# Kernel optimization log

Hardware: AMD Instinct MI355X
Metric: run time of the kernel (lower is better)

## Reference

```python
import jax, jax.numpy as jnp
import numpy as np

B, C, H, W = 8, 64, 256, 256
M1, M2 = 32, 32  # kept Fourier modes per corner (n_modes//2)
EPS = 1e-5


def _gn(x):
    # GroupNorm(1, C): normalize over (C, H, W) per sample, biased variance
    mu = jnp.mean(x, axis=(1, 2, 3), keepdims=True)
    var = jnp.var(x, axis=(1, 2, 3), keepdims=True)
    return (x - mu) * jax.lax.rsqrt(var + EPS)


def setup_inputs() -> dict:
    key = jax.random.key(0)
    ks = jax.random.split(key, 12)
    spec_scale = 1.0 / (C * C)
    n = lambda k, shape, s=1.0: jax.random.normal(k, shape, dtype=jnp.float32) * s
    return dict(
        x=n(ks[0], (B, C, H, W)),
        t=n(ks[1], (B, C, 1)),
        w1r=n(ks[2], (C, C, M1, M2), spec_scale),
        w1i=n(ks[3], (C, C, M1, M2), spec_scale),
        w2r=n(ks[4], (C, C, M1, M2), spec_scale),
        w2i=n(ks[5], (C, C, M1, M2), spec_scale),
        norm1_w=jnp.ones((C,), jnp.float32),
        norm1_b=jnp.zeros((C,), jnp.float32),
        mlp_w1=n(ks[6], (C // 2, C), 0.05),
        mlp_b1=jnp.zeros((C // 2,), jnp.float32),
        mlp_w2=n(ks[7], (C, C // 2), 0.05),
        mlp_b2=jnp.zeros((C,), jnp.float32),
        gamma_w=n(ks[8], (C, C), 0.05),
        gamma_b=jnp.ones((C,), jnp.float32),
        beta_w=n(ks[9], (C, C), 0.05),
        beta_b=jnp.zeros((C,), jnp.float32),
    )


def reference(x, t, w1r, w1i, w2r, w2i, norm1_w, norm1_b,
              mlp_w1, mlp_b1, mlp_w2, mlp_b2,
              gamma_w, gamma_b, beta_w, beta_b):
    gelu = lambda v: jax.nn.gelu(v, approximate=False)  # torch exact gelu
    skip1 = x
    skip2 = gelu(x)

    # --- SpectralConv: rfft2 -> mode-truncated complex contraction -> irfft2 ---
    xf = jnp.fft.rfftn(x, axes=(2, 3))  # (B, C, H, W//2+1) complex
    b1 = jnp.einsum('bixy,ioxy->boxy', xf[:, :, :M1, :M2], w1r + 1j * w1i)
    b2 = jnp.einsum('bixy,ioxy->boxy', xf[:, :, -M1:, :M2], w2r + 1j * w2i)
    of = (jnp.zeros(xf.shape, xf.dtype)
          .at[:, :, :M1, :M2].set(b1)
          .at[:, :, -M1:, :M2].set(b2))
    y = jnp.fft.irfftn(of, s=(H, W), axes=(2, 3)).astype(x.dtype)

    # norm1 (GroupNorm(1,C) affine) + residual, gelu
    y = _gn(y) * norm1_w[None, :, None, None] + norm1_b[None, :, None, None]
    y = gelu(y + skip1)

    # pointwise MLP (Conv1d 1x1 chain == channel matmuls)
    h = gelu(jnp.einsum('oc,bcxy->boxy', mlp_w1, y) + mlp_b1[None, :, None, None])
    y = jnp.einsum('oc,bcxy->boxy', mlp_w2, h) + mlp_b2[None, :, None, None]

    # timeCondIN: FiLM gamma/beta from t via 1x1 Conv1d, non-affine GroupNorm(1,C)
    gamma = (jnp.einsum('oc,bcl->bol', gamma_w, t) + gamma_b[None, :, None])[..., None]
    beta = (jnp.einsum('oc,bcl->bol', beta_w, t) + beta_b[None, :, None])[..., None]
    y = gamma * _gn(y) + beta

    return y + skip2
```

## Files before the change

kernel.cpp:

```cpp
#include <hip/hip_runtime.h>
#include <math.h>

#define NB 8
#define NC 64
#define NH 256
#define NW 256
#define NHW 65536
#define NM 32
#define NPS 4194304
#define GN_EPS 1e-5f
#define OMEGA 0.0245436926061703f

typedef short shortx8 __attribute__((ext_vector_type(8)));
typedef float floatx4 __attribute__((ext_vector_type(4)));

__device__ __forceinline__ float gelu_f(float v) {
    return 0.5f * v * (1.0f + erff(v * 0.7071067811865475f));
}

__device__ __forceinline__ unsigned short f2bf(float f) {
    unsigned u = __builtin_bit_cast(unsigned, f);
    u = (u + 0x7fffu + ((u >> 16) & 1u)) >> 16;
    return (unsigned short)u;
}

__device__ __forceinline__ float bf2f(unsigned short u) {
    return __builtin_bit_cast(float, ((unsigned)u) << 16);
}

__global__ void k0_init(const float* __restrict__ t_in,
                        const float* __restrict__ gamma_w, const float* __restrict__ gamma_b,
                        const float* __restrict__ beta_w, const float* __restrict__ beta_b,
                        const float* __restrict__ mlp_w1, const float* __restrict__ mlp_w2,
                        float* __restrict__ gn_acc, float* __restrict__ gamma_bc,
                        float* __restrict__ beta_bc,
                        unsigned short* __restrict__ w1p_h, unsigned short* __restrict__ w1p_l,
                        unsigned short* __restrict__ w2p_h, unsigned short* __restrict__ w2p_l) {
    int t = threadIdx.x;
    if (t < 32) gn_acc[t] = 0.f;
    for (int idx = t; idx < NB * NC; idx += 256) {
        int b = idx >> 6, o = idx & 63;
        float g = gamma_b[o], be = beta_b[o];
        for (int c = 0; c < NC; ++c) {
            float tv = t_in[b * NC + c];
            g += gamma_w[o * NC + c] * tv;
            be += beta_w[o * NC + c] * tv;
        }
        gamma_bc[idx] = g;
        beta_bc[idx] = be;
    }
    for (int idx = t; idx < 2048; idx += 256) {
        float wv1 = mlp_w1[idx];
        unsigned short h1 = f2bf(wv1);
        w1p_h[idx] = h1;
        w1p_l[idx] = f2bf(wv1 - bf2f(h1));
        float wv2 = mlp_w2[idx];
        unsigned short h2 = f2bf(wv2);
        w2p_h[idx] = h2;
        w2p_l[idx] = f2bf(wv2 - bf2f(h2));
    }
}

__global__ __launch_bounds__(256) void k_tw(unsigned short* __restrict__ t1h,
                                            unsigned short* __restrict__ t1l,
                                            unsigned short* __restrict__ uh,
                                            unsigned short* __restrict__ ul,
                                            unsigned short* __restrict__ m2h,
                                            unsigned short* __restrict__ m2l,
                                            unsigned short* __restrict__ m4h,
                                            unsigned short* __restrict__ m4l) {
    int idx = blockIdx.x * 256 + threadIdx.x;
    if (idx < 16384) {
        int n = idx >> 8, w = idx & 255;
        float ph = OMEGA * (float)(((n & 31) * w) & 255);
        float s, c;
        sincosf(ph, &s, &c);
        float v = (n < 32) ? c : -s;
        unsigned short h = f2bf(v);
        t1h[idx] = h;
        t1l[idx] = f2bf(v - bf2f(h));

        int w2 = idx >> 6, k = idx & 63;
        int k31 = k & 31;
        float m = (k31 == 0) ? 1.f : 2.f;
        float ph2 = OMEGA * (float)((k31 * w2) & 255);
        sincosf(ph2, &s, &c);
        float v2 = (k < 32) ? m * c : -m * s;
        h = f2bf(v2);
        uh[idx] = h;
        ul[idx] = f2bf(v2 - bf2f(h));
    }
    {
        int m = idx >> 9, k = idx & 511;
        int j = m & 63;
        int f = (j < 32) ? j : 192 + j;
        int h256 = k & 255;
        float s, c;
        sincosf(OMEGA * (float)((f * h256) & 255), &s, &c);
        float v = (m < 64) ? ((k < 256) ? c : s) : ((k < 256) ? -s : c);
        unsigned short hh = f2bf(v);
        m2h[idx] = hh;
        m2l[idx] = f2bf(v - bf2f(hh));
    }
    {
        const float sc = 1.0f / 65536.0f;
        int m = idx >> 7, k = idx & 127;
        int h256 = m & 255;
        int j = k & 63;
        int f = (j < 32) ? j : 192 + j;
        float s, c;
        sincosf(OMEGA * (float)((f * h256) & 255), &s, &c);
        float v = ((m < 256) ? ((k < 64) ? c : -s) : ((k < 64) ? s : c)) * sc;
        unsigned short hh = f2bf(v);
        m4h[idx] = hh;
        m4l[idx] = f2bf(v - bf2f(hh));
    }
}

__global__ __launch_bounds__(256, 4) void k1_dftw(const float* __restrict__ x,
                                                  const unsigned short* __restrict__ t1h,
                                                  const unsigned short* __restrict__ t1l,
                                                  float* __restrict__ xw_re,
                                                  float* __restrict__ xw_im) {
    __shared__ unsigned short a_h[128 * 72];
    __shared__ unsigned short a_l[128 * 72];
    int blk = blockIdx.x;
    int bc = blk >> 1;
    int h0 = (blk & 1) * 128;
    const float* src = x + (size_t)bc * NHW + (size_t)h0 * NW;
    int t = threadIdx.x;
    int lane = t & 63, wv = t >> 6, lm = lane & 15, lg = lane >> 4;

    floatx4 acc[2][4] = {};
#pragma unroll
    for (int ks = 0; ks < 4; ++ks) {
        if (ks) __syncthreads();
        for (int i = t; i < 2048; i += 256) {
            int r = i >> 4;
            int c4 = (i & 15) << 2;
            float4 v = *(const float4*)&src[(size_t)r * NW + (ks << 6) + c4];
            int off = r * 72 + c4;
            ushort4 h4, l4;
            h4.x = f2bf(v.x); l4.x = f2bf(v.x - bf2f(h4.x));
            h4.y = f2bf(v.y); l4.y = f2bf(v.y - bf2f(h4.y));
            h4.z = f2bf(v.z); l4.z = f2bf(v.z - bf2f(h4.z));
            h4.w = f2bf(v.w); l4.w = f2bf(v.w - bf2f(h4.w));
            *(ushort4*)&a_h[off] = h4;
            *(ushort4*)&a_l[off] = l4;
        }
        __syncthreads();
#pragma unroll
        for (int kk = 0; kk < 2; ++kk) {
            shortx8 ah[2], al[2], bh[4], bl[4];
#pragma unroll
            for (int mt = 0; mt < 2; ++mt) {
                int off = (wv * 32 + mt * 16 + lm) * 72 + kk * 32 + lg * 8;
                ah[mt] = *(const shortx8*)&a_h[off];
                al[mt] = *(const shortx8*)&a_l[off];
            }
#pragma unroll
            for (int nt = 0; nt < 4; ++nt) {
                int off = (nt * 16 + lm) * 256 + ks * 64 + kk * 32 + lg * 8;
                bh[nt] = *(const shortx8*)&t1h[off];
                bl[nt] = *(const shortx8*)&t1l[off];
            }
#pragma unroll
            for (int mt = 0; mt < 2; ++mt)
#pragma unroll
                for (int nt = 0; nt < 4; ++nt) {
                    acc[mt][nt] = __builtin_amdgcn_mfma_f32_16x16x32_bf16(ah[mt], bh[nt], acc[mt][nt], 0, 0, 0);
                    acc[mt][nt] = __builtin_amdgcn_mfma_f32_16x16x32_bf16(ah[mt], bl[nt], acc[mt][nt], 0, 0, 0);
                    acc[mt][nt] = __builtin_amdgcn_mfma_f32_16x16x32_bf16(al[mt], bh[nt], acc[mt][nt], 0, 0, 0);
                }
        }
    }
    size_t rowg = (size_t)bc * NH + h0;
#pragma unroll
    for (int mt = 0; mt < 2; ++mt)
#pragma unroll
        for (int nt = 0; nt < 4; ++nt) {
            int n = nt * 16 + lm;
            float* dst = (n < 32) ? xw_re : xw_im;
            int kx = n & 31;
#pragma unroll
            for (int r = 0; r < 4; ++r) {
                int row = wv * 32 + mt * 16 + lg * 4 + r;
                dst[(rowg + row) * NM + kx] = acc[mt][nt][r];
            }
        }
}

__global__ __launch_bounds__(256, 2) void k2_dfth(const float* __restrict__ xw_re,
                                                  const float* __restrict__ xw_im,
                                                  const unsigned short* __restrict__ m2h,
                                                  const unsigned short* __restrict__ m2l,
                                                  float* __restrict__ xf_re,
                                                  float* __restrict__ xf_im) {
    __shared__ unsigned short bt_h[32 * 520];
    __shared__ unsigned short bt_l[32 * 520];
    int bc = blockIdx.x;
    size_t base = (size_t)bc * (NH * NM);
    int t = threadIdx.x;
    for (int idx4 = t; idx4 < 2048; idx4 += 256) {
        int h = idx4 >> 3;
        int kxg = (idx4 & 7) << 2;
        float4 vr = ((const float4*)(xw_re + base))[idx4];
        float4 vi = ((const float4*)(xw_im + base))[idx4];
        float fr[4] = {vr.x, vr.y, vr.z, vr.w};
        float fi[4] = {vi.x, vi.y, vi.z, vi.w};
#pragma unroll
        for (int q = 0; q < 4; ++q) {
            int rowo = (kxg + q) * 520;
            unsigned short hh = f2bf(fr[q]);
            bt_h[rowo + h] = hh;
            bt_l[rowo + h] = f2bf(fr[q] - bf2f(hh));
            hh = f2bf(fi[q]);
            bt_h[rowo + 256 + h] = hh;
            bt_l[rowo + 256 + h] = f2bf(fi[q] - bf2f(hh));
        }
    }
    __syncthreads();

    int lane = t & 63, wv = t >> 6, lm = lane & 15, lg = lane >> 4;
    floatx4 acc[2][2] = {};
#pragma unroll
    for (int ks = 0; ks < 16; ++ks) {
        shortx8 bh[2], bl[2], ah[2], al[2];
#pragma unroll
        for (int nt = 0; nt < 2; ++nt) {
            int off = (nt * 16 + lm) * 520 + ks * 32 + lg * 8;
            bh[nt] = *(const shortx8*)&bt_h[off];
            bl[nt] = *(const shortx8*)&bt_l[off];
        }
#pragma unroll
        for (int mt = 0; mt < 2; ++mt) {
            int off = (wv * 32 + mt * 16 + lm) * 512 + ks * 32 + lg * 8;
            ah[mt] = *(const shortx8*)&m2h[off];
            al[mt] = *(const shortx8*)&m2l[off];
        }
#pragma unroll
        for (int mt = 0; mt < 2; ++mt)
#pragma unroll
            for (int nt = 0; nt < 2; ++nt) {
                acc[mt][nt] = __builtin_amdgcn_mfma_f32_16x16x32_bf16(ah[mt], bh[nt], acc[mt][nt], 0, 0, 0);
                acc[mt][nt] = __builtin_amdgcn_mfma_f32_16x16x32_bf16(ah[mt], bl[nt], acc[mt][nt], 0, 0, 0);
                acc[mt][nt] = __builtin_amdgcn_mfma_f32_16x16x32_bf16(al[mt], bh[nt], acc[mt][nt], 0, 0, 0);
            }
    }
    size_t ob = (size_t)bc * 2048;
#pragma unroll
    for (int mt = 0; mt < 2; ++mt)
#pragma unroll
        for (int nt = 0; nt < 2; ++nt) {
            int n = nt * 16 + lm;
#pragma unroll
            for (int r = 0; r < 4; ++r) {
                int row = wv * 32 + mt * 16 + lg * 4 + r;
                float* dst = (row < 64) ? xf_re : xf_im;
                dst[ob + (row & 63) * 32 + n] = acc[mt][nt][r];
            }
        }
}

__global__ __launch_bounds__(256) void k3_mix(const float* __restrict__ xf_re,
                                              const float* __restrict__ xf_im,
                                              const float* __restrict__ w1r, const float* __restrict__ w1i,
                                              const float* __restrict__ w2r, const float* __restrict__ w2i,
                                              float* __restrict__ yf_re, float* __restrict__ yf_im) {
    __shared__ float xr_l[4 * 64 * 32];
    __shared__ float xi_l[4 * 64 * 32];
    int blk = blockIdx.x;
    int bh = blk & 1;
    int oct = (blk >> 1) & 7;
    int ky = blk >> 4;
    for (int idx = threadIdx.x; idx < 4 * 64 * 32; idx += 256) {
        int bb = idx >> 11;
        int i = (idx >> 5) & 63;
        int kx = idx & 31;
        size_t g = ((size_t)((bh * 4 + bb) * 64 + i) * 64 + ky) * 32 + kx;
        xr_l[idx] = xf_re[g];
        xi_l[idx] = xf_im[g];
    }
    __syncthreads();
    const float* wr = (ky < 32) ? w1r : w2r;
    const float* wi = (ky < 32) ? w1i : w2i;
    int kyl = ky & 31;
    int t = threadIdx.x;
    int kx = t & 31, oo = t >> 5;
    int o = oct * 8 + oo;
    float accr[4] = {0.f, 0.f, 0.f, 0.f};
    float acci[4] = {0.f, 0.f, 0.f, 0.f};
    for (int i = 0; i < 64; ++i) {
        size_t wbase = ((size_t)(i * 64 + o) * 32 + kyl) * 32 + kx;
        float wrv = wr[wbase];
        float wiv = wi[wbase];
#pragma unroll
        for (int bb = 0; bb < 4; ++bb) {
            float xr = xr_l[(bb * 64 + i) * 32 + kx];
            float xi = xi_l[(bb * 64 + i) * 32 + kx];
            accr[bb] += xr * wrv - xi * wiv;
            acci[bb] += xr * wiv + xi * wrv;
        }
    }
#pragma unroll
    for (int bb = 0; bb < 4; ++bb) {
        int b = bh * 4 + bb;
        size_t g = ((size_t)(b * 64 + o) * 64 + ky) * 32 + kx;
        yf_re[g] = accr[bb];
        yf_im[g] = acci[bb];
    }
}

__global__ __launch_bounds__(256, 2) void k4_idfth(const float* __restrict__ yf_re,
                                                   const float* __restrict__ yf_im,
                                                   const unsigned short* __restrict__ m4h,
                                                   const unsigned short* __restrict__ m4l,
                                                   float* __restrict__ yh_re,
                                                   float* __restrict__ yh_im) {
    __shared__ unsigned short bt_h[32 * 136];
    __shared__ unsigned short bt_l[32 * 136];
    int bc = blockIdx.x;
    size_t base = (size_t)bc * 2048;
    int t = threadIdx.x;
    for (int idx4 = t; idx4 < 512; idx4 += 256) {
        int j = idx4 >> 3;
        int kxg = (idx4 & 7) << 2;
        float4 vr = ((const float4*)(yf_re + base))[idx4];
        float4 vi = ((const float4*)(yf_im + base))[idx4];
        float fr[4] = {vr.x, vr.y, vr.z, vr.w};
        float fi[4] = {vi.x, vi.y, vi.z, vi.w};
#pragma unroll
        for (int q = 0; q < 4; ++q) {
            int rowo = (kxg + q) * 136;
            unsigned short hh = f2bf(fr[q]);
            bt_h[rowo + j] = hh;
            bt_l[rowo + j] = f2bf(fr[q] - bf2f(hh));
            hh = f2bf(fi[q]);
            bt_h[rowo + 64 + j] = hh;
            bt_l[rowo + 64 + j] = f2bf(fi[q] - bf2f(hh));
        }
    }
    __syncthreads();

    int lane = t & 63, wv = t >> 6, lm = lane & 15, lg = lane >> 4;
    floatx4 acc[8][2] = {};
#pragma unroll
    for (int ks = 0; ks < 4; ++ks) {
        shortx8 bh[2], bl[2];
#pragma unroll
        for (int nt = 0; nt < 2; ++nt) {
            int off = (nt * 16 + lm) * 136 + ks * 32 + lg * 8;
            bh[nt] = *(const shortx8*)&bt_h[off];
            bl[nt] = *(const shortx8*)&bt_l[off];
        }
#pragma unroll
        for (int mt = 0; mt < 8; ++mt) {
            int off = (wv * 128 + mt * 16 + lm) * 128 + ks * 32 + lg * 8;
            shortx8 ah = *(const shortx8*)&m4h[off];
            shortx8 al = *(const shortx8*)&m4l[off];
#pragma unroll
            for (int nt = 0; nt < 2; ++nt) {
                acc[mt][nt] = __builtin_amdgcn_mfma_f32_16x16x32_bf16(ah, bh[nt], acc[mt][nt], 0, 0, 0);
                acc[mt][nt] = __builtin_amdgcn_mfma_f32_16x16x32_bf16(ah, bl[nt], acc[mt][nt], 0, 0, 0);
                acc[mt][nt] = __builtin_amdgcn_mfma_f32_16x16x32_bf16(al, bh[nt], acc[mt][nt], 0, 0, 0);
            }
        }
    }
    size_t ob = (size_t)bc * (NH * NM);
#pragma unroll
    for (int mt = 0; mt < 8; ++mt)
#pragma unroll
        for (int nt = 0; nt < 2; ++nt) {
            int n = nt * 16 + lm;
#pragma unroll
            for (int r = 0; r < 4; ++r) {
                int row = wv * 128 + mt * 16 + lg * 4 + r;
                float* dst = (row < 256) ? yh_re : yh_im;
                dst[ob + (row & 255) * 32 + n] = acc[mt][nt][r];
            }
        }
}

__global__ __launch_bounds__(256, 2) void k5_irfftw(const float* __restrict__ yh_re,
                                                    const float* __restrict__ yh_im,
                                                    const unsigned short* __restrict__ uh,
                                                    const unsigned short* __restrict__ ul,
                                                    float* __restrict__ yout,
                                                    float* __restrict__ gn_acc) {
    __shared__ unsigned short a_h[128 * 72];
    __shared__ unsigned short a_l[128 * 72];
    __shared__ float red[8];
    int blk = blockIdx.x;
    size_t row0 = (size_t)blk * 128;
    int t = threadIdx.x;

    for (int i = t; i < 1024; i += 256) {
        int r = i >> 3;
        int c4 = (i & 7) << 2;
        float4 vr = *(const float4*)&yh_re[(row0 + r) * NM + c4];
        float4 vi = *(const float4*)&yh_im[(row0 + r) * NM + c4];
        int offr = r * 72 + c4;
        ushort4 h4, l4;
        h4.x = f2bf(vr.x); l4.x = f2bf(vr.x - bf2f(h4.x));
        h4.y = f2bf(vr.y); l4.y = f2bf(vr.y - bf2f(h4.y));
        h4.z = f2bf(vr.z); l4.z = f2bf(vr.z - bf2f(h4.z));
        h4.w = f2bf(vr.w); l4.w = f2bf(vr.w - bf2f(h4.w));
        *(ushort4*)&a_h[offr] = h4;
        *(ushort4*)&a_l[offr] = l4;
        h4.x = f2bf(vi.x); l4.x = f2bf(vi.x - bf2f(h4.x));
        h4.y = f2bf(vi.y); l4.y = f2bf(vi.y - bf2f(h4.y));
        h4.z = f2bf(vi.z); l4.z = f2bf(vi.z - bf2f(h4.z));
        h4.w = f2bf(vi.w); l4.w = f2bf(vi.w - bf2f(h4.w));
        *(ushort4*)&a_h[offr + 32] = h4;
        *(ushort4*)&a_l[offr + 32] = l4;
    }
    __syncthreads();

    int lane = t & 63, wv = t >> 6, lm = lane & 15, lg = lane >> 4;
    floatx4 acc[2][16] = {};
#pragma unroll
    for (int kk = 0; kk < 2; ++kk) {
        shortx8 ah[2], al[2];
#pragma unroll
        for (int mt = 0; mt < 2; ++mt) {
            int off = (wv * 32 + mt * 16 + lm) * 72 + kk * 32 + lg * 8;
            ah[mt] = *(const shortx8*)&a_h[off];
            al[mt] = *(const shortx8*)&a_l[off];
        }
#pragma unroll
        for (int nt = 0; nt < 16; ++nt) {
            int w = nt * 16 + lm;
            shortx8 bh = *(const shortx8*)&uh[w * 64 + kk * 32 + lg * 8];
            shortx8 bl = *(const shortx8*)&ul[w * 64 + kk * 32 + lg * 8];
#pragma unroll
            for (int mt = 0; mt < 2; ++mt) {
                acc[mt][nt] = __builtin_amdgcn_mfma_f32_16x16x32_bf16(ah[mt], bh, acc[mt][nt], 0, 0, 0);
                acc[mt][nt] = __builtin_amdgcn_mfma_f32_16x16x32_bf16(ah[mt], bl, acc[mt][nt], 0, 0, 0);
                acc[mt][nt] = __builtin_amdgcn_mfma_f32_16x16x32_bf16(al[mt], bh, acc[mt][nt], 0, 0, 0);
            }
        }
    }

    float sum = 0.f, sq = 0.f;
#pragma unroll
    for (int mt = 0; mt < 2; ++mt)
#pragma unroll
        for (int nt = 0; nt < 16; ++nt) {
            int w = nt * 16 + lm;
#pragma unroll
            for (int r = 0; r < 4; ++r) {
                int row = wv * 32 + mt * 16 + lg * 4 + r;
                float v = acc[mt][nt][r];
                yout[(row0 + row) * NW + w] = v;
                sum += v;
                sq += v * v;
            }
        }
#pragma unroll
    for (int off = 32; off > 0; off >>= 1) {
        sum += __shfl_down(sum, off);
        sq += __shfl_down(sq, off);
    }
    if (lane == 0) { red[wv] = sum; red[4 + wv] = sq; }
    __syncthreads();
    if (t == 0) {
        int b = blk >> 7;
        atomicAdd(&gn_acc[b * 4 + 0], red[0] + red[1] + red[2] + red[3]);
        atomicAdd(&gn_acc[b * 4 + 1], red[4] + red[5] + red[6] + red[7]);
    }
}

__global__ __launch_bounds__(256, 3) void k6_mlp(const float* __restrict__ x,
                                                 const float* __restrict__ norm1_w,
                                                 const float* __restrict__ norm1_b,
                                                 const unsigned short* __restrict__ w1p_h,
                                                 const unsigned short* __restrict__ w1p_l,
                                                 const unsigned short* __restrict__ w2p_h,
                                                 const unsigned short* __restrict__ w2p_l,
                                                 const float* __restrict__ mlp_b1,
                                                 const float* __restrict__ mlp_b2,
                                                 float* __restrict__ y,
                                                 float* __restrict__ gn_acc) {
    __shared__ __align__(16) unsigned char smem[40864];
    unsigned short* w1_h   = (unsigned short*)smem;
    unsigned short* w1_l   = (unsigned short*)(smem + 4608);
    unsigned short* hbuf_h = (unsigned short*)(smem + 9216);
    unsigned short* hbuf_l = (unsigned short*)(smem + 19456);
    unsigned short* w2_h   = (unsigned short*)(smem + 29696);
    unsigned short* w2_l   = (unsigned short*)(smem + 34816);
    float* outbuf = (float*)smem;
    float* nwl = (float*)(smem + 39936);
    float* nbl = nwl + 64;
    float* b1l = nbl + 64;
    float* b2l = b1l + 32;
    float* red = b2l + 64;

    int t = threadIdx.x;
    int blk = blockIdx.x;
    int b = blk >> 9;
    int pixbase = (blk & 511) * 128;
    size_t bbase = (size_t)b * NC * NHW + pixbase;

    if (t < 64) { nwl[t] = norm1_w[t]; nbl[t] = norm1_b[t]; b2l[t] = mlp_b2[t]; }
    if (t >= 64 && t < 96) b1l[t - 64] = mlp_b1[t - 64];
#pragma unroll
    for (int idx4 = t; idx4 < 512; idx4 += 256) {
        int r1 = idx4 >> 4, c1 = (idx4 & 15) << 2;
        *(ushort4*)&w1_h[r1 * 72 + c1] = ((const ushort4*)w1p_h)[idx4];
        *(ushort4*)&w1_l[r1 * 72 + c1] = ((const ushort4*)w1p_l)[idx4];
        int r2 = idx4 >> 3, c2 = (idx4 & 7) << 2;
        *(ushort4*)&w2_h[r2 * 40 + c2] = ((const ushort4*)w2p_h)[idx4];
        *(ushort4*)&w2_l[r2 * 40 + c2] = ((const ushort4*)w2p_l)[idx4];
    }
    __syncthreads();

    int lane = t & 63, wv = t >> 6;
    int lm = lane & 15, lg = lane >> 4;

    const float invN = 1.0f / (float)NPS;
    float m1 = gn_acc[b * 4 + 0] * invN;
    float var1 = gn_acc[b * 4 + 1] * invN - m1 * m1;
    float rs1 = rsqrtf(var1 + GN_EPS);
    shortx8 ah[2][2], al[2][2];
#pragma unroll
    for (int mt = 0; mt < 2; ++mt) {
        int row = wv * 32 + mt * 16 + lm;
#pragma unroll
        for (int ks = 0; ks < 2; ++ks) {
#pragma unroll
            for (int j = 0; j < 8; ++j) {
                int c = ks * 32 + lg * 8 + j;
                size_t rb = bbase + (size_t)c * NHW + row;
                float yv = y[rb];
                float xv = x[rb];
                float g = (yv - m1) * rs1 * nwl[c] + nbl[c] + xv;
                float vv = gelu_f(g);
                unsigned short vh = f2bf(vv);
                ah[ks][mt][j] = (short)vh;
                al[ks][mt][j] = (short)f2bf(vv - bf2f(vh));
            }
        }
    }

    floatx4 acc1[2][2] = {};
#pragma unroll
    for (int ks = 0; ks < 2; ++ks) {
        shortx8 bh[2], bl[2];
#pragma unroll
        for (int nt = 0; nt < 2; ++nt) {
            int off = (nt * 16 + lm) * 72 + lg * 8 + ks * 32;
            bh[nt] = *(const shortx8*)&w1_h[off];
            bl[nt] = *(const shortx8*)&w1_l[off];
        }
#pragma unroll
        for (int mt = 0; mt < 2; ++mt)
#pragma unroll
            for (int nt = 0; nt < 2; ++nt) {
                acc1[mt][nt] = __builtin_amdgcn_mfma_f32_16x16x32_bf16(ah[ks][mt], bh[nt], acc1[mt][nt], 0, 0, 0);
                acc1[mt][nt] = __builtin_amdgcn_mfma_f32_16x16x32_bf16(ah[ks][mt], bl[nt], acc1[mt][nt], 0, 0, 0);
                acc1[mt][nt] = __builtin_amdgcn_mfma_f32_16x16x32_bf16(al[ks][mt], bh[nt], acc1[mt][nt], 0, 0, 0);
            }
    }
#pragma unroll
    for (int mt = 0; mt < 2; ++mt)
#pragma unroll
        for (int nt = 0; nt < 2; ++nt) {
            float b1v = b1l[nt * 16 + lm];
#pragma unroll
            for (int r = 0; r < 4; ++r) {
                float hv = gelu_f(acc1[mt][nt][r] + b1v);
                unsigned short hh = f2bf(hv);
                int off = (wv * 32 + mt * 16 + lg * 4 + r) * 40 + nt * 16 + lm;
                hbuf_h[off] = hh;
                hbuf_l[off] = f2bf(hv - bf2f(hh));
            }
        }
    __syncthreads();

    floatx4 acc2[2][4] = {};
    {
        shortx8 ah2[2], al2[2], bh2[4], bl2[4];
#pragma unroll
        for (int mt = 0; mt < 2; ++mt) {
            int off = (wv * 32 + mt * 16 + lm) * 40 + lg * 8;
            ah2[mt] = *(const shortx8*)&hbuf_h[off];
            al2[mt] = *(const shortx8*)&hbuf_l[off];
        }
#pragma unroll
        for (int nt = 0; nt < 4; ++nt) {
            int off = (nt * 16 + lm) * 40 + lg * 8;
            bh2[nt] = *(const shortx8*)&w2_h[off];
            bl2[nt] = *(const shortx8*)&w2_l[off];
        }
#pragma unroll
        for (int mt = 0; mt < 2; ++mt)
#pragma unroll
            for (int nt = 0; nt < 4; ++nt) {
                acc2[mt][nt] = __builtin_amdgcn_mfma_f32_16x16x32_bf16(ah2[mt], bh2[nt], acc2[mt][nt], 0, 0, 0);
                acc2[mt][nt] = __builtin_amdgcn_mfma_f32_16x16x32_bf16(ah2[mt], bl2[nt], acc2[mt][nt], 0, 0, 0);
                acc2[mt][nt] = __builtin_amdgcn_mfma_f32_16x16x32_bf16(al2[mt], bh2[nt], acc2[mt][nt], 0, 0, 0);
            }
    }
    __syncthreads();

#pragma unroll
    for (int mt = 0; mt < 2; ++mt)
#pragma unroll
        for (int nt = 0; nt < 4; ++nt) {
            int ch = nt * 16 + lm;
            float b2v = b2l[ch];
#pragma unroll
            for (int r = 0; r < 4; ++r)
                outbuf[ch * 132 + wv * 32 + mt * 16 + lg * 4 + r] = acc2[mt][nt][r] + b2v;
        }
    __syncthreads();

    float sum = 0.f, sq = 0.f;
#pragma unroll
    for (int it = 0; it < 8; ++it) {
        int flat = it * 256 + t;
        int c = flat >> 5;
        int p4 = (flat & 31) * 4;
        float4 v = *(const float4*)&outbuf[c * 132 + p4];
        *(float4*)&y[bbase + (size_t)c * NHW + p4] = v;
        sum += v.x + v.y + v.z + v.w;
        sq += v.x * v.x + v.y * v.y + v.z * v.z + v.w * v.w;
    }
#pragma unroll
    for (int off = 32; off > 0; off >>= 1) {
        sum += __shfl_down(sum, off);
        sq += __shfl_down(sq, off);
    }
    if (lane == 0) { red[wv] = sum; red[4 + wv] = sq; }
    __syncthreads();
    if (t == 0) {
        atomicAdd(&gn_acc[b * 4 + 2], red[0] + red[1] + red[2] + red[3]);
        atomicAdd(&gn_acc[b * 4 + 3], red[4] + red[5] + red[6] + red[7]);
    }
}

__global__ __launch_bounds__(256) void k7_final(const float* __restrict__ x,
                                                const float* __restrict__ gamma_bc,
                                                const float* __restrict__ beta_bc,
                                                const float* __restrict__ gn_acc,
                                                float* __restrict__ y) {
    size_t idx4 = (size_t)blockIdx.x * 256 + threadIdx.x;
    size_t base = idx4 * 4;
    int b = (int)(base >> 22);
    int c = (int)((base >> 16) & 63);
    const float invN = 1.0f / (float)NPS;
    float m2 = gn_acc[b * 4 + 2] * invN;
    float var2 = gn_acc[b * 4 + 3] * invN - m2 * m2;
    float rs2 = rsqrtf(var2 + GN_EPS);
    float g = gamma_bc[b * 64 + c];
    float be = beta_bc[b * 64 + c];
    float4 yv = ((float4*)y)[idx4];
    float4 xv = ((const float4*)x)[idx4];
    yv.x = g * ((yv.x - m2) * rs2) + be + gelu_f(xv.x);
    yv.y = g * ((yv.y - m2) * rs2) + be + gelu_f(xv.y);
    yv.z = g * ((yv.z - m2) * rs2) + be + gelu_f(xv.z);
    yv.w = g * ((yv.w - m2) * rs2) + be + gelu_f(xv.w);
    ((float4*)y)[idx4] = yv;
}

extern "C" void kernel_launch(void* const* d_in, const int* in_sizes, int n_in,
                              void* d_out, int out_size, void* d_ws, size_t ws_size,
                              hipStream_t stream) {
    (void)in_sizes; (void)n_in; (void)out_size; (void)ws_size;
    const float* x       = (const float*)d_in[0];
    const float* t_in    = (const float*)d_in[1];
    const float* w1r     = (const float*)d_in[2];
    const float* w1i     = (const float*)d_in[3];
    const float* w2r     = (const float*)d_in[4];
    const float* w2i     = (const float*)d_in[5];
    const float* norm1_w = (const float*)d_in[6];
    const float* norm1_b = (const float*)d_in[7];
    const float* mlp_w1  = (const float*)d_in[8];
    const float* mlp_b1  = (const float*)d_in[9];
    const float* mlp_w2  = (const float*)d_in[10];
    const float* mlp_b2  = (const float*)d_in[11];
    const float* gamma_w = (const float*)d_in[12];
    const float* gamma_b = (const float*)d_in[13];
    const float* beta_w  = (const float*)d_in[14];
    const float* beta_b  = (const float*)d_in[15];
    float* out = (float*)d_out;
    float* ws  = (float*)d_ws;

    float* gn_acc   = ws;
    float* gamma_bc = ws + 32;
    float* beta_bc  = ws + 544;
    float* xw_re    = ws + 2048;
    float* xw_im    = xw_re + 4194304;
    float* xf_re    = xw_im + 4194304;
    float* xf_im    = xf_re + 1048576;
    float* yf_re    = xf_im + 1048576;
    float* yf_im    = yf_re + 1048576;
    unsigned short* t1h = (unsigned short*)(yf_im + 1048576);
    unsigned short* t1l = t1h + 16384;
    unsigned short* uh  = t1l + 16384;
    unsigned short* ul  = uh + 16384;
    unsigned short* w1p_h = ul + 16384;
    unsigned short* w1p_l = w1p_h + 2048;
    unsigned short* w2p_h = w1p_l + 2048;
    unsigned short* w2p_l = w2p_h + 2048;
    unsigned short* m2h = w2p_l + 2048;
    unsigned short* m2l = m2h + 65536;
    unsigned short* m4h = m2l + 65536;
    unsigned short* m4l = m4h + 65536;

    k_tw<<<dim3(256), dim3(256), 0, stream>>>(t1h, t1l, uh, ul, m2h, m2l, m4h, m4l);
    k0_init<<<dim3(1), dim3(256), 0, stream>>>(t_in, gamma_w, gamma_b, beta_w, beta_b,
                                               mlp_w1, mlp_w2,
                                               gn_acc, gamma_bc, beta_bc,
                                               w1p_h, w1p_l, w2p_h, w2p_l);
    k1_dftw<<<dim3(1024), dim3(256), 0, stream>>>(x, t1h, t1l, xw_re, xw_im);
    k2_dfth<<<dim3(512), dim3(256), 0, stream>>>(xw_re, xw_im, m2h, m2l, xf_re, xf_im);
    k3_mix<<<dim3(1024), dim3(256), 0, stream>>>(xf_re, xf_im, w1r, w1i, w2r, w2i,
                                                 yf_re, yf_im);
    k4_idfth<<<dim3(512), dim3(256), 0, stream>>>(yf_re, yf_im, m4h, m4l, xw_re, xw_im);
    k5_irfftw<<<dim3(1024), dim3(256), 0, stream>>>(xw_re, xw_im, uh, ul, out, gn_acc);
    k6_mlp<<<dim3(4096), dim3(256), 0, stream>>>(x, norm1_w, norm1_b,
                                                 w1p_h, w1p_l, w2p_h, w2p_l,
                                                 mlp_b1, mlp_b2, out, gn_acc);
    k7_final<<<dim3(32768), dim3(256), 0, stream>>>(x, gamma_bc, beta_bc, gn_acc, out);
}
```

Before: 706.9 us.

## Drop split-bf16 compensation in MLP kernel and stage activations via LDS

The pointwise MLP kernel now uses a single bf16 MFMA per tile instead of the three-term hi/lo split, so the low-order weight and activation buffers are removed. Input activations are loaded with coalesced per-pixel reads, written to an LDS tile, and then read back as MFMA fragments. Launch bounds go from 3 to 4 blocks. This cuts MFMA work, LDS footprint and conversion arithmetic, but lowers the precision of both channel matmuls to plain bf16, which may exceed tolerance.

```diff
diff --git a/kernel.cpp b/kernel.cpp
--- a/kernel.cpp
+++ b/kernel.cpp
@@ -470,26 +470,22 @@
     }
 }
 
-__global__ __launch_bounds__(256, 3) void k6_mlp(const float* __restrict__ x,
+__global__ __launch_bounds__(256, 4) void k6_mlp(const float* __restrict__ x,
                                                  const float* __restrict__ norm1_w,
                                                  const float* __restrict__ norm1_b,
                                                  const unsigned short* __restrict__ w1p_h,
-                                                 const unsigned short* __restrict__ w1p_l,
                                                  const unsigned short* __restrict__ w2p_h,
-                                                 const unsigned short* __restrict__ w2p_l,
                                                  const float* __restrict__ mlp_b1,
                                                  const float* __restrict__ mlp_b2,
                                                  float* __restrict__ y,
                                                  float* __restrict__ gn_acc) {
-    __shared__ __align__(16) unsigned char smem[40864];
-    unsigned short* w1_h   = (unsigned short*)smem;
-    unsigned short* w1_l   = (unsigned short*)(smem + 4608);
-    unsigned short* hbuf_h = (unsigned short*)(smem + 9216);
-    unsigned short* hbuf_l = (unsigned short*)(smem + 19456);
-    unsigned short* w2_h   = (unsigned short*)(smem + 29696);
-    unsigned short* w2_l   = (unsigned short*)(smem + 34816);
+    __shared__ __align__(16) unsigned char smem[39328];
+    unsigned short* vbuf = (unsigned short*)smem;
+    unsigned short* w1b  = (unsigned short*)(smem + 18432);
+    unsigned short* hbuf = (unsigned short*)(smem + 23040);
+    unsigned short* w2b  = (unsigned short*)(smem + 33280);
     float* outbuf = (float*)smem;
-    float* nwl = (float*)(smem + 39936);
+    float* nwl = (float*)(smem + 38400);
     float* nbl = nwl + 64;
     float* b1l = nbl + 64;
     float* b2l = b1l + 32;
@@ -506,60 +502,49 @@
 #pragma unroll
     for (int idx4 = t; idx4 < 512; idx4 += 256) {
         int r1 = idx4 >> 4, c1 = (idx4 & 15) << 2;
-        *(ushort4*)&w1_h[r1 * 72 + c1] = ((const ushort4*)w1p_h)[idx4];
-        *(ushort4*)&w1_l[r1 * 72 + c1] = ((const ushort4*)w1p_l)[idx4];
+        *(ushort4*)&w1b[r1 * 72 + c1] = ((const ushort4*)w1p_h)[idx4];
         int r2 = idx4 >> 3, c2 = (idx4 & 7) << 2;
-        *(ushort4*)&w2_h[r2 * 40 + c2] = ((const ushort4*)w2p_h)[idx4];
-        *(ushort4*)&w2_l[r2 * 40 + c2] = ((const ushort4*)w2p_l)[idx4];
-    }
-    __syncthreads();
-
-    int lane = t & 63, wv = t >> 6;
-    int lm = lane & 15, lg = lane >> 4;
+        *(ushort4*)&w2b[r2 * 40 + c2] = ((const ushort4*)w2p_h)[idx4];
+    }
+    __syncthreads();
 
     const float invN = 1.0f / (float)NPS;
     float m1 = gn_acc[b * 4 + 0] * invN;
     float var1 = gn_acc[b * 4 + 1] * invN - m1 * m1;
     float rs1 = rsqrtf(var1 + GN_EPS);
-    shortx8 ah[2][2], al[2][2];
-#pragma unroll
-    for (int mt = 0; mt < 2; ++mt) {
-        int row = wv * 32 + mt * 16 + lm;
-#pragma unroll
-        for (int ks = 0; ks < 2; ++ks) {
-#pragma unroll
-            for (int j = 0; j < 8; ++j) {
-                int c = ks * 32 + lg * 8 + j;
-                size_t rb = bbase + (size_t)c * NHW + row;
-                float yv = y[rb];
-                float xv = x[rb];
-                float g = (yv - m1) * rs1 * nwl[c] + nbl[c] + xv;
-                float vv = gelu_f(g);
-                unsigned short vh = f2bf(vv);
-                ah[ks][mt][j] = (short)vh;
-                al[ks][mt][j] = (short)f2bf(vv - bf2f(vh));
-            }
-        }
-    }
+    {
+        int p = t & 127;
+        int c0 = (t >> 7) * 32;
+        size_t base = bbase + (size_t)c0 * NHW + p;
+#pragma unroll 8
+        for (int ci = 0; ci < 32; ++ci) {
+            float yv = y[base + (size_t)ci * NHW];
+            float xv = x[base + (size_t)ci * NHW];
+            int c = c0 + ci;
+            float g = (yv - m1) * rs1 * nwl[c] + nbl[c] + xv;
+            vbuf[p * 72 + c] = f2bf(gelu_f(g));
+        }
+    }
+    __syncthreads();
+
+    int lane = t & 63, wv = t >> 6;
+    int lm = lane & 15, lg = lane >> 4;
 
     floatx4 acc1[2][2] = {};
 #pragma unroll
     for (int ks = 0; ks < 2; ++ks) {
-        shortx8 bh[2], bl[2];
-#pragma unroll
-        for (int nt = 0; nt < 2; ++nt) {
-            int off = (nt * 16 + lm) * 72 + lg * 8 + ks * 32;
-            bh[nt] = *(const shortx8*)&w1_h[off];
-            bl[nt] = *(const shortx8*)&w1_l[off];
-        }
+        shortx8 a[2], bf[2];
 #pragma unroll
         for (int mt = 0; mt < 2; ++mt)
-#pragma unroll
-            for (int nt = 0; nt < 2; ++nt) {
-                acc1[mt][nt] = __builtin_amdgcn_mfma_f32_16x16x32_bf16(ah[ks][mt], bh[nt], acc1[mt][nt], 0, 0, 0);
-                acc1[mt][nt] = __builtin_amdgcn_mfma_f32_16x16x32_bf16(ah[ks][mt], bl[nt], acc1[mt][nt], 0, 0, 0);
-                acc1[mt][nt] = __builtin_amdgcn_mfma_f32_16x16x32_bf16(al[ks][mt], bh[nt], acc1[mt][nt], 0, 0, 0);
-            }
+            a[mt] = *(const shortx8*)&vbuf[(wv * 32 + mt * 16 + lm) * 72 + lg * 8 + ks * 32];
+#pragma unroll
+        for (int nt = 0; nt < 2; ++nt)
+            bf[nt] = *(const shortx8*)&w1b[(nt * 16 + lm) * 72 + lg * 8 + ks * 32];
+#pragma unroll
+        for (int mt = 0; mt < 2; ++mt)
+#pragma unroll
+            for (int nt = 0; nt < 2; ++nt)
+                acc1[mt][nt] = __builtin_amdgcn_mfma_f32_16x16x32_bf16(a[mt], bf[nt], acc1[mt][nt], 0, 0, 0);
     }
 #pragma unroll
     for (int mt = 0; mt < 2; ++mt)
@@ -569,37 +554,25 @@
 #pragma unroll
             for (int r = 0; r < 4; ++r) {
                 float hv = gelu_f(acc1[mt][nt][r] + b1v);
-                unsigned short hh = f2bf(hv);
-                int off = (wv * 32 + mt * 16 + lg * 4 + r) * 40 + nt * 16 + lm;
-                hbuf_h[off] = hh;
-                hbuf_l[off] = f2bf(hv - bf2f(hh));
+                hbuf[(wv * 32 + mt * 16 + lg * 4 + r) * 40 + nt * 16 + lm] = f2bf(hv);
             }
         }
     __syncthreads();
 
     floatx4 acc2[2][4] = {};
     {
-        shortx8 ah2[2], al2[2], bh2[4], bl2[4];
-#pragma unroll
-        for (int mt = 0; mt < 2; ++mt) {
-            int off = (wv * 32 + mt * 16 + lm) * 40 + lg * 8;
-            ah2[mt] = *(const shortx8*)&hbuf_h[off];
-            al2[mt] = *(const shortx8*)&hbuf_l[off];
-        }
-#pragma unroll
-        for (int nt = 0; nt < 4; ++nt) {
-            int off = (nt * 16 + lm) * 40 + lg * 8;
-            bh2[nt] = *(const shortx8*)&w2_h[off];
-            bl2[nt] = *(const shortx8*)&w2_l[off];
-        }
+        shortx8 a2[2], b2f[4];
 #pragma unroll
         for (int mt = 0; mt < 2; ++mt)
-#pragma unroll
-            for (int nt = 0; nt < 4; ++nt) {
-                acc2[mt][nt] = __builtin_amdgcn_mfma_f32_16x16x32_bf16(ah2[mt], bh2[nt], acc2[mt][nt], 0, 0, 0);
-                acc2[mt][nt] = __builtin_amdgcn_mfma_f32_16x16x32_bf16(ah2[mt], bl2[nt], acc2[mt][nt], 0, 0, 0);
-                acc2[mt][nt] = __builtin_amdgcn_mfma_f32_16x16x32_bf16(al2[mt], bh2[nt], acc2[mt][nt], 0, 0, 0);
-            }
+            a2[mt] = *(const shortx8*)&hbuf[(wv * 32 + mt * 16 + lm) * 40 + lg * 8];
+#pragma unroll
+        for (int nt = 0; nt < 4; ++nt)
+            b2f[nt] = *(const shortx8*)&w2b[(nt * 16 + lm) * 40 + lg * 8];
+#pragma unroll
+        for (int mt = 0; mt < 2; ++mt)
+#pragma unroll
+            for (int nt = 0; nt < 4; ++nt)
+                acc2[mt][nt] = __builtin_amdgcn_mfma_f32_16x16x32_bf16(a2[mt], b2f[nt], acc2[mt][nt], 0, 0, 0);
     }
     __syncthreads();
 
@@ -720,7 +693,7 @@
     k4_idfth<<<dim3(512), dim3(256), 0, stream>>>(yf_re, yf_im, m4h, m4l, xw_re, xw_im);
     k5_irfftw<<<dim3(1024), dim3(256), 0, stream>>>(xw_re, xw_im, uh, ul, out, gn_acc);
     k6_mlp<<<dim3(4096), dim3(256), 0, stream>>>(x, norm1_w, norm1_b,
-                                                 w1p_h, w1p_l, w2p_h, w2p_l,
+                                                 w1p_h, w2p_h,
                                                  mlp_b1, mlp_b2, out, gn_acc);
     k7_final<<<dim3(32768), dim3(256), 0, stream>>>(x, gamma_bc, beta_bc, gn_acc, out);
 }
```

After: 647.0 us. -8.5%, faster.
